# Optimization experiments

Measured on AMD Instinct MI355X. Metric: run time of the kernel, lower is better.

The kernel has to match this reference:

```python
import jax, jax.numpy as jnp
import numpy as np

N = 50000      # nodes
E = 1_600_000  # edges (avg degree 32)
H = 32         # hidden_dim
ED = 16        # edge_dim
L = 4          # num EGNN layers
F_IN = 23      # prot_in_dim
LN_EPS = 1e-5


def setup_inputs() -> dict:
    key = jax.random.key(0)
    ks = jax.random.split(key, 24)
    s = 0.1  # param init scale
    inp = {
        "node_pos": jax.random.normal(ks[0], (N, 3), jnp.float32) * 10.0,
        "node_feat": jax.random.normal(ks[1], (N, F_IN), jnp.float32),
        "edge_attr": jax.random.normal(ks[2], (E, ED), jnp.float32),
        "proj_w": jax.random.normal(ks[3], (F_IN, H), jnp.float32) * s,
        "proj_b": jnp.zeros((H,), jnp.float32),
        # phi_e: Linear(2H+ED+1 -> H), SiLU, Linear(H -> H)   [stacked over L layers]
        "pe_w1": jax.random.normal(ks[4], (L, 2 * H + ED + 1, H), jnp.float32) * s,
        "pe_b1": jnp.zeros((L, H), jnp.float32),
        "pe_w2": jax.random.normal(ks[5], (L, H, H), jnp.float32) * s,
        "pe_b2": jnp.zeros((L, H), jnp.float32),
        # phi_h: Linear(2H -> H), SiLU, Linear(H -> H)
        "ph_w1": jax.random.normal(ks[6], (L, 2 * H, H), jnp.float32) * s,
        "ph_b1": jnp.zeros((L, H), jnp.float32),
        "ph_w2": jax.random.normal(ks[7], (L, H, H), jnp.float32) * s,
        "ph_b2": jnp.zeros((L, H), jnp.float32),
        # phi_x: Linear(H -> H), SiLU, Linear(H -> 1)
        "px_w1": jax.random.normal(ks[8], (L, H, H), jnp.float32) * s,
        "px_b1": jnp.zeros((L, H), jnp.float32),
        "px_w2": jax.random.normal(ks[9], (L, H, 1), jnp.float32) * s,
        "px_b2": jnp.zeros((L, 1), jnp.float32),
        # LayerNorm per layer
        "ln_g": jnp.ones((L, H), jnp.float32),
        "ln_b": jnp.zeros((L, H), jnp.float32),
        "edge_index": jax.random.randint(ks[10], (2, E), 0, N, dtype=jnp.int32),
    }
    return inp


def _mlp2(x, w1, b1, w2, b2):
    # Linear -> SiLU -> Linear (dropout=0 / eval mode)
    return jax.nn.silu(x @ w1 + b1) @ w2 + b2


def _layernorm(x, g, b):
    mu = jnp.mean(x, axis=-1, keepdims=True)
    var = jnp.mean(jnp.square(x - mu), axis=-1, keepdims=True)
    return (x - mu) * jax.lax.rsqrt(var + LN_EPS) * g + b


def reference(node_pos, node_feat, edge_attr, proj_w, proj_b,
              pe_w1, pe_b1, pe_w2, pe_b2,
              ph_w1, ph_b1, ph_w2, ph_b2,
              px_w1, px_b1, px_w2, px_b2,
              ln_g, ln_b, edge_index):
    src = edge_index[0]
    dst = edge_index[1]
    n = node_feat.shape[0]

    h = node_feat @ proj_w + proj_b  # (N,H)
    x = node_pos                     # (N,3)

    for l in range(L):
        h_i = h[src]                 # (E,H)
        h_j = h[dst]                 # (E,H)
        x_i = x[src]                 # (E,3)
        x_j = x[dst]                 # (E,3)
        diff = x_j - x_i             # (E,3)
        dist = jnp.sqrt(jnp.sum(diff * diff, axis=-1, keepdims=True) + 1e-09)  # (E,1)

        m_in = jnp.concatenate([h_i, h_j, edge_attr, dist], axis=-1)  # (E, 2H+ED+1)
        m_ij = _mlp2(m_in, pe_w1[l], pe_b1[l], pe_w2[l], pe_b2[l])    # (E,H)

        agg = jax.ops.segment_sum(m_ij, dst, num_segments=n)          # (N,H)
        dh = _mlp2(jnp.concatenate([h, agg], axis=-1),
                   ph_w1[l], ph_b1[l], ph_w2[l], ph_b2[l])            # (N,H)
        h = _layernorm(h + dh, ln_g[l], ln_b[l])

        # coordinate update: x_j += sum_i unit(x_j - x_i) * phi_x(m_ij)
        dir_norm = jnp.linalg.norm(diff, axis=-1, keepdims=True) + 1e-09
        gate = _mlp2(m_ij, px_w1[l], px_b1[l], px_w2[l], px_b2[l])    # (E,1)
        coord_msg = (diff / dir_norm) * gate                          # (E,3)
        dx = jax.ops.segment_sum(coord_msg, dst, num_segments=n)      # (N,3)
        x = x + dx

    return h, x
```

## Files before the change

### kernel.cpp

```cpp
#include <hip/hip_runtime.h>
#include <hip/hip_fp16.h>
#include <math.h>

#define NN 50000
#define NE 1600000
#define H  32
#define ED 16
#define FIN 23
#define NL 4
#define W1ROWS 81
#define CPAD 16
#define LW 19

typedef _Float16 hv2 __attribute__((ext_vector_type(2)));
typedef __fp16   fv2 __attribute__((ext_vector_type(2)));
union H2U { unsigned int u; hv2 h; fv2 f; };
union F4 { float4 v; float f[4]; };

__device__ __forceinline__ unsigned int pack2(float a, float b) {
    H2U r; r.f = __builtin_amdgcn_cvt_pkrtz(a, b);
    return r.u;
}

__device__ __forceinline__ float fdot2f(unsigned int a, unsigned int b, float c) {
    H2U ua, ub; ua.u = a; ub.u = b;
    return __builtin_amdgcn_fdot2(ua.h, ub.h, c, false);
}

__device__ __forceinline__ float silu_f(float v) {
    float e = __expf(-v);
    return v * __builtin_amdgcn_rcpf(1.0f + e);
}

__device__ __forceinline__ void acc4(float hid[H], float4 hv4, const float* __restrict__ w) {
    F4 u; u.v = hv4;
    #pragma unroll
    for (int jj = 0; jj < 4; ++jj) {
        float v = u.f[jj];
        #pragma unroll
        for (int k = 0; k < H; ++k) hid[k] = fmaf(v, w[jj * H + k], hid[k]);
    }
}


__global__ __launch_bounds__(256) void k_prep(
    const float* __restrict__ pe_w1, const float* __restrict__ pe_w2,
    const float* __restrict__ pe_b2,
    const float* __restrict__ px_w1, const float* __restrict__ px_b1,
    unsigned int* __restrict__ w1h, unsigned int* __restrict__ w2xh,
    float* __restrict__ cvec)
{
    __shared__ float w2x[H * H];
    int l = blockIdx.x;
    const float* w2  = pe_w2 + (size_t)l * H * H;
    const float* xw1 = px_w1 + (size_t)l * H * H;
    int tid = threadIdx.x;
    #pragma unroll
    for (int q = 0; q < 4; ++q) {
        int idx = q * 256 + tid;
        int j = idx >> 5, k = idx & 31;
        float acc = 0.0f;
        #pragma unroll
        for (int t = 0; t < H; ++t) acc = fmaf(w2[j * H + t], xw1[t * H + k], acc);
        w2x[idx] = acc;
    }
    __syncthreads();
    #pragma unroll
    for (int q = 0; q < 2; ++q) {
        int i2 = q * 256 + tid;
        int j2 = i2 >> 5, k = i2 & 31;
        w2xh[(size_t)l * 512 + i2] = pack2(w2x[(2*j2) * H + k], w2x[(2*j2+1) * H + k]);
    }
    {
        int j2 = tid >> 5, k = tid & 31;
        const float* w1 = pe_w1 + (size_t)l * W1ROWS * H;
        w1h[(size_t)l * 256 + tid] = pack2(w1[(2*H + 2*j2) * H + k], w1[(2*H + 2*j2+1) * H + k]);
    }
    if (tid < H) {
        float acc = px_b1[l * H + tid];
        const float* b2 = pe_b2 + l * H;
        #pragma unroll
        for (int t = 0; t < H; ++t) acc = fmaf(b2[t], xw1[t * H + tid], acc);
        cvec[l * H + tid] = acc;
    }
}


__global__ __launch_bounds__(256) void k_hist(
    const int* __restrict__ edst, int* __restrict__ cnt, int* __restrict__ rank)
{
    int e = blockIdx.x * 256 + threadIdx.x;
    if (e >= NE) return;
    rank[e] = atomicAdd(&cnt[(size_t)edst[e] * CPAD], 1);
}

__global__ __launch_bounds__(1024) void k_scan(
    const int* __restrict__ cnt, int* __restrict__ rs)
{
    __shared__ int wsum[16];
    __shared__ int s_carry;
    int t = threadIdx.x;
    int lane = t & 63, wid = t >> 6;
    if (t == 0) s_carry = 0;
    __syncthreads();
    for (int base = 0; base < NN; base += 1024) {
        int i = base + t;
        int v = (i < NN) ? cnt[(size_t)i * CPAD] : 0;
        int incl = v;
        #pragma unroll
        for (int off = 1; off < 64; off <<= 1) {
            int u = __shfl_up(incl, off, 64);
            if (lane >= off) incl += u;
        }
        if (lane == 63) wsum[wid] = incl;
        __syncthreads();
        int wpre = 0;
        #pragma unroll
        for (int w = 0; w < 16; ++w) { int ws = wsum[w]; wpre += (w < wid) ? ws : 0; }
        int carry = s_carry;
        if (i < NN) rs[i] = carry + wpre + incl - v;
        __syncthreads();
        if (t == 1023) s_carry = carry + wpre + incl;
        __syncthreads();
    }
    if (t == 0) rs[NN] = s_carry;
}

__global__ __launch_bounds__(256) void k_scatter2(
    const int* __restrict__ esrc, const int* __restrict__ edst,
    const int* __restrict__ rank, const int* __restrict__ rs,
    const float* __restrict__ ea,
    unsigned int* __restrict__ ea_h, unsigned int* __restrict__ sdp)
{
    int e = blockIdx.x * 256 + threadIdx.x;
    if (e >= NE) return;
    int s = esrc[e], d = edst[e];
    int slot = rs[d] + rank[e];
    const float4* src4 = (const float4*)(ea + (size_t)e * ED);
    uint2* dst2 = (uint2*)(ea_h + (size_t)slot * 8);
    #pragma unroll
    for (int j = 0; j < ED / 4; ++j) {
        float4 v = src4[j];
        uint2 o; o.x = pack2(v.x, v.y); o.y = pack2(v.z, v.w);
        dst2[j] = o;
    }
    sdp[slot] = (unsigned int)s | ((unsigned int)d << 16);
}


__global__ __launch_bounds__(256) void proj2(
    const float* __restrict__ feat, const float* __restrict__ pos,
    const float* __restrict__ W, const float* __restrict__ bias,
    const float* __restrict__ pew1,
    float* __restrict__ h, float* __restrict__ a, float* __restrict__ b,
    float4* __restrict__ xp)
{
    int n = blockIdx.x * 256 + threadIdx.x;
    if (n >= NN) return;
    float acc[H];
    #pragma unroll
    for (int k = 0; k < H; ++k) acc[k] = bias[k];
    #pragma unroll 1
    for (int j = 0; j < FIN; ++j) {
        float v = feat[n * FIN + j];
        const float* w = W + j * H;
        #pragma unroll
        for (int k = 0; k < H; ++k) acc[k] = fmaf(v, w[k], acc[k]);
    }
    float4* h4 = (float4*)(h + (size_t)n * H);
    #pragma unroll
    for (int k4 = 0; k4 < H / 4; ++k4) {
        float4 o;
        o.x = acc[4*k4+0]; o.y = acc[4*k4+1]; o.z = acc[4*k4+2]; o.w = acc[4*k4+3];
        h4[k4] = o;
    }
    float pa[H];
    #pragma unroll
    for (int k = 0; k < H; ++k) pa[k] = 0.0f;
    #pragma unroll 1
    for (int j = 0; j < H; ++j) {
        float v = acc[j];
        const float* w = pew1 + j * H;
        #pragma unroll
        for (int k = 0; k < H; ++k) pa[k] = fmaf(v, w[k], pa[k]);
    }
    float4* a4 = (float4*)(a + (size_t)n * H);
    #pragma unroll
    for (int k4 = 0; k4 < H / 4; ++k4) {
        float4 o;
        o.x = pa[4*k4+0]; o.y = pa[4*k4+1]; o.z = pa[4*k4+2]; o.w = pa[4*k4+3];
        a4[k4] = o;
    }
    #pragma unroll
    for (int k = 0; k < H; ++k) pa[k] = 0.0f;
    #pragma unroll 1
    for (int j = 0; j < H; ++j) {
        float v = acc[j];
        const float* w = pew1 + (H + j) * H;
        #pragma unroll
        for (int k = 0; k < H; ++k) pa[k] = fmaf(v, w[k], pa[k]);
    }
    float4* b4 = (float4*)(b + (size_t)n * H);
    #pragma unroll
    for (int k4 = 0; k4 < H / 4; ++k4) {
        float4 o;
        o.x = pa[4*k4+0]; o.y = pa[4*k4+1]; o.z = pa[4*k4+2]; o.w = pa[4*k4+3];
        b4[k4] = o;
    }
    float4 xo;
    xo.x = pos[3*n+0]; xo.y = pos[3*n+1]; xo.z = pos[3*n+2]; xo.w = 0.0f;
    xp[n] = xo;
}


__global__ __launch_bounds__(256) void egnn_edge6(
    const float* __restrict__ a, const float* __restrict__ b,
    const float4* __restrict__ xp,
    const unsigned int* __restrict__ ea_h, const unsigned int* __restrict__ sdp,
    const unsigned int* __restrict__ w1h, const float* __restrict__ b1,
    const float* __restrict__ w1,
    const unsigned int* __restrict__ w2xh, const float* __restrict__ cvec,
    const float* __restrict__ xw2, const float* __restrict__ xb2,
    float* __restrict__ agg, float* __restrict__ dxb)
{
    __shared__ unsigned int ldsu[256 * LW + 4];

    int tid = threadIdx.x;
    int w = tid >> 6, lane = tid & 63;
    int slot = blockIdx.x * 256 + tid;

    unsigned int sd = sdp[slot];
    int s = (int)(sd & 0xffffu), d = (int)(sd >> 16);

    float hid[H];
    const float4* av = (const float4*)(a + (size_t)s * H);
    const float4* bv = (const float4*)(b + (size_t)d * H);
    #pragma unroll
    for (int k4 = 0; k4 < H / 4; ++k4) {
        F4 ua, ub; ua.v = av[k4]; ub.v = bv[k4];
        #pragma unroll
        for (int jj = 0; jj < 4; ++jj)
            hid[4*k4+jj] = b1[4*k4+jj] + ua.f[jj] + ub.f[jj];
    }

    const uint4* ev = (const uint4*)(ea_h + (size_t)slot * 8);
    uint4 e0 = ev[0], e1 = ev[1];
    unsigned int ew[8] = { e0.x, e0.y, e0.z, e0.w, e1.x, e1.y, e1.z, e1.w };
    #pragma unroll 1
    for (int j2 = 0; j2 < 8; ++j2) {
        unsigned int ea2 = ew[j2];
        const unsigned int* wr = w1h + j2 * H;
        #pragma unroll
        for (int k = 0; k < H; ++k) hid[k] = fdot2f(ea2, wr[k], hid[k]);
    }

    float4 xi = xp[s];
    float4 xj = xp[d];
    float d0 = xj.x - xi.x, d1 = xj.y - xi.y, d2 = xj.z - xi.z;
    float sq = d0*d0 + d1*d1 + d2*d2;
    float dist = __builtin_amdgcn_sqrtf(sq + 1e-9f);
    {
        const float* wl = w1 + (2 * H + ED) * H;
        #pragma unroll
        for (int k = 0; k < H; ++k) hid[k] = fmaf(dist, wl[k], hid[k]);
    }

    unsigned int sp[16];
    #pragma unroll
    for (int j2 = 0; j2 < 16; ++j2)
        sp[j2] = pack2(silu_f(hid[2*j2]), silu_f(hid[2*j2+1]));

    float gh[H];
    #pragma unroll
    for (int k = 0; k < H; ++k) gh[k] = cvec[k];
    #pragma unroll 1
    for (int j2 = 0; j2 < 16; ++j2) {
        unsigned int sv = sp[j2];
        const unsigned int* wr = w2xh + j2 * H;
        #pragma unroll
        for (int k = 0; k < H; ++k) gh[k] = fdot2f(sv, wr[k], gh[k]);
    }

    float gate = xb2[0];
    #pragma unroll
    for (int j = 0; j < H; ++j) gate = fmaf(silu_f(gh[j]), xw2[j], gate);
    float scale = gate * __builtin_amdgcn_rcpf(__builtin_amdgcn_sqrtf(sq) + 1e-9f);

    unsigned int* row = &ldsu[tid * LW];
    #pragma unroll
    for (int k2 = 0; k2 < 16; ++k2) row[k2] = sp[k2];
    row[16] = __float_as_uint(d0 * scale);
    row[17] = __float_as_uint(d1 * scale);
    row[18] = __float_as_uint(d2 * scale);

    int dprev = __shfl_up(d, 1, 64);
    bool flag = (lane == 0) || (d != dprev);
    unsigned long long ball = __ballot(flag);

    int half = lane >> 5, col = lane & 31;
    int word = col >> 1, sh = (col & 1) * 16;
    int c = lane & 3, strip = lane >> 2;
    const unsigned int* wrows = &ldsu[(w * 64) * LW];

    unsigned long long cur = ball;
    while (cur) {
        int r0 = (int)__builtin_ctzll(cur);
        unsigned long long nxt = cur & (cur - 1);
        int r1 = nxt ? (int)__builtin_ctzll(nxt) : 64;
        int dseg = __shfl(d, r0, 64);

        float v = 0.0f;
        #pragma unroll 1
        for (int r = r0 + half; r < r1; r += 2) {
            unsigned int u = wrows[r * LW + word];
            v += __half2float(__ushort_as_half((unsigned short)(u >> sh)));
        }
        v += __shfl_xor(v, 32, 64);
        if (lane < 32) unsafeAtomicAdd(&agg[(size_t)dseg * H + col], v);

        float cv = 0.0f;
        #pragma unroll 1
        for (int r = r0 + strip; r < r1; r += 16)
            cv += __uint_as_float(wrows[r * LW + 16 + c]);
        cv += __shfl_xor(cv, 4, 64);
        cv += __shfl_xor(cv, 8, 64);
        cv += __shfl_xor(cv, 16, 64);
        cv += __shfl_xor(cv, 32, 64);
        if (lane < 3) unsafeAtomicAdd(&dxb[(size_t)dseg * 4 + c], cv);

        cur = nxt;
    }
}


__global__ __launch_bounds__(256) void egnn_node6(
    const float* __restrict__ h, float* __restrict__ agg,
    const float4* __restrict__ xin, float* __restrict__ dxb,
    const int* __restrict__ rs,
    const float* __restrict__ ew2, const float* __restrict__ eb2,
    const float* __restrict__ w1, const float* __restrict__ b1,
    const float* __restrict__ w2, const float* __restrict__ b2,
    const float* __restrict__ lng, const float* __restrict__ lnb,
    const float* __restrict__ nxtw1, int last,
    float* __restrict__ hout, float* __restrict__ xout,
    float* __restrict__ aout, float* __restrict__ bout)
{
    int n = blockIdx.x * 256 + threadIdx.x;
    if (n >= NN) return;
    const float4* h4 = (const float4*)(h + (size_t)n * H);
    float4* a4 = (float4*)(agg + (size_t)n * H);

    float degf = (float)(rs[n + 1] - rs[n]);
    float ma[H];
    #pragma unroll
    for (int k = 0; k < H; ++k) ma[k] = degf * eb2[k];
    #pragma unroll 1
    for (int j4 = 0; j4 < H / 4; ++j4)
        acc4(ma, a4[j4], ew2 + (j4 * 4) * H);

    float4 z; z.x = 0.0f; z.y = 0.0f; z.z = 0.0f; z.w = 0.0f;
    #pragma unroll
    for (int j4 = 0; j4 < H / 4; ++j4) a4[j4] = z;

    float hv[H];
    float hid[H];
    #pragma unroll
    for (int k = 0; k < H; ++k) hid[k] = b1[k];
    #pragma unroll 1
    for (int j4 = 0; j4 < H / 4; ++j4) {
        F4 u; u.v = h4[j4];
        #pragma unroll
        for (int jj = 0; jj < 4; ++jj) hv[4*j4+jj] = u.f[jj];
        acc4(hid, u.v, w1 + (j4 * 4) * H);
    }
    #pragma unroll
    for (int j = 0; j < H; ++j) {
        float v = ma[j];
        const float* ww = w1 + (H + j) * H;
        #pragma unroll
        for (int k = 0; k < H; ++k) hid[k] = fmaf(v, ww[k], hid[k]);
    }

    float dh[H];
    #pragma unroll
    for (int k = 0; k < H; ++k) dh[k] = b2[k];
    #pragma unroll
    for (int j = 0; j < H; ++j) {
        float v = silu_f(hid[j]);
        const float* ww = w2 + j * H;
        #pragma unroll
        for (int k = 0; k < H; ++k) dh[k] = fmaf(v, ww[k], dh[k]);
    }

    float y[H];
    float mu = 0.0f;
    #pragma unroll
    for (int k = 0; k < H; ++k) { y[k] = hv[k] + dh[k]; mu += y[k]; }
    mu *= (1.0f / H);
    float var = 0.0f;
    #pragma unroll
    for (int k = 0; k < H; ++k) { float t = y[k] - mu; var += t * t; }
    var *= (1.0f / H);
    float rstd = rsqrtf(var + 1e-5f);

    float hn[H];
    #pragma unroll
    for (int k = 0; k < H; ++k) hn[k] = (y[k] - mu) * rstd * lng[k] + lnb[k];

    float4* ho4 = (float4*)(hout + (size_t)n * H);
    #pragma unroll
    for (int k4 = 0; k4 < H / 4; ++k4) {
        float4 o;
        o.x = hn[4*k4+0]; o.y = hn[4*k4+1]; o.z = hn[4*k4+2]; o.w = hn[4*k4+3];
        ho4[k4] = o;
    }

    float4 xi = xin[n];
    float nx0 = xi.x + dxb[(size_t)n * 4 + 0];
    float nx1 = xi.y + dxb[(size_t)n * 4 + 1];
    float nx2 = xi.z + dxb[(size_t)n * 4 + 2];
    ((float4*)dxb)[n] = z;
    if (last) {
        xout[3*n+0] = nx0; xout[3*n+1] = nx1; xout[3*n+2] = nx2;
    } else {
        float4 o; o.x = nx0; o.y = nx1; o.z = nx2; o.w = 0.0f;
        ((float4*)xout)[n] = o;
    }

    if (!last) {
        float pa[H];
        #pragma unroll
        for (int k = 0; k < H; ++k) pa[k] = 0.0f;
        #pragma unroll 1
        for (int j = 0; j < H; ++j) {
            float v = hn[j];
            const float* ww = nxtw1 + j * H;
            #pragma unroll
            for (int k = 0; k < H; ++k) pa[k] = fmaf(v, ww[k], pa[k]);
        }
        float4* ao4 = (float4*)(aout + (size_t)n * H);
        #pragma unroll
        for (int k4 = 0; k4 < H / 4; ++k4) {
            float4 o;
            o.x = pa[4*k4+0]; o.y = pa[4*k4+1]; o.z = pa[4*k4+2]; o.w = pa[4*k4+3];
            ao4[k4] = o;
        }
        #pragma unroll
        for (int k = 0; k < H; ++k) pa[k] = 0.0f;
        #pragma unroll 1
        for (int j = 0; j < H; ++j) {
            float v = hn[j];
            const float* ww = nxtw1 + (H + j) * H;
            #pragma unroll
            for (int k = 0; k < H; ++k) pa[k] = fmaf(v, ww[k], pa[k]);
        }
        float4* bo4 = (float4*)(bout + (size_t)n * H);
        #pragma unroll
        for (int k4 = 0; k4 < H / 4; ++k4) {
            float4 o;
            o.x = pa[4*k4+0]; o.y = pa[4*k4+1]; o.z = pa[4*k4+2]; o.w = pa[4*k4+3];
            bo4[k4] = o;
        }
    }
}

extern "C" void kernel_launch(void* const* d_in, const int* in_sizes, int n_in,
                              void* d_out, int out_size, void* d_ws, size_t ws_size,
                              hipStream_t stream) {
    const float* node_pos  = (const float*)d_in[0];
    const float* node_feat = (const float*)d_in[1];
    const float* edge_attr = (const float*)d_in[2];
    const float* proj_w    = (const float*)d_in[3];
    const float* proj_b    = (const float*)d_in[4];
    const float* pe_w1     = (const float*)d_in[5];
    const float* pe_b1     = (const float*)d_in[6];
    const float* pe_w2     = (const float*)d_in[7];
    const float* pe_b2     = (const float*)d_in[8];
    const float* ph_w1     = (const float*)d_in[9];
    const float* ph_b1     = (const float*)d_in[10];
    const float* ph_w2     = (const float*)d_in[11];
    const float* ph_b2     = (const float*)d_in[12];
    const float* px_w1     = (const float*)d_in[13];
    const float* px_b1     = (const float*)d_in[14];
    const float* px_w2     = (const float*)d_in[15];
    const float* px_b2     = (const float*)d_in[16];
    const float* ln_g      = (const float*)d_in[17];
    const float* ln_b      = (const float*)d_in[18];
    const int*   eidx      = (const int*)d_in[19];
    const int*   esrc      = eidx;
    const int*   edst      = eidx + NE;

    float* out_h = (float*)d_out;
    float* out_x = out_h + (size_t)NN * H;

    size_t off = 0;
    unsigned int* ea_h = (unsigned int*)d_ws;   off += (size_t)NE * 8;
    unsigned int* sdp = (unsigned int*)((float*)d_ws + off); off += NE;
    float* abuf = (float*)d_ws + off;          off += (size_t)NN * H;
    float* bbuf = (float*)d_ws + off;          off += (size_t)NN * H;
    float* h_a  = (float*)d_ws + off;          off += (size_t)NN * H;
    float* h_b  = (float*)d_ws + off;          off += (size_t)NN * H;
    float4* xp_a = (float4*)((float*)d_ws + off); off += (size_t)NN * 4;
    float4* xp_b = (float4*)((float*)d_ws + off); off += (size_t)NN * 4;
    float* agg  = (float*)d_ws + off;          off += (size_t)NN * H;
    float* dxb  = (float*)d_ws + off;          off += (size_t)NN * 4;
    unsigned int* w1h  = (unsigned int*)((float*)d_ws + off); off += (size_t)NL * 256;
    unsigned int* w2xh = (unsigned int*)((float*)d_ws + off); off += (size_t)NL * 512;
    float* cvec = (float*)d_ws + off;          off += (size_t)NL * H;
    int*   cnt  = (int*)((float*)d_ws + off);  off += (size_t)NN * CPAD;
    int*   rs   = (int*)((float*)d_ws + off);  off += NN + 4;
    int*   rank = (int*)((float*)d_ws + off);  off += NE;

    dim3 nblk((NN + 255) / 256), eblk(NE / 256);

    hipMemsetAsync(cnt, 0, (size_t)NN * CPAD * sizeof(int), stream);
    hipMemsetAsync(agg, 0, (size_t)NN * (H + 4) * sizeof(float), stream);
    k_hist<<<eblk, 256, 0, stream>>>(edst, cnt, rank);
    k_scan<<<1, 1024, 0, stream>>>(cnt, rs);
    k_scatter2<<<eblk, 256, 0, stream>>>(esrc, edst, rank, rs, edge_attr, ea_h, sdp);
    k_prep<<<dim3(NL), 256, 0, stream>>>(pe_w1, pe_w2, pe_b2, px_w1, px_b1, w1h, w2xh, cvec);

    proj2<<<nblk, 256, 0, stream>>>(node_feat, node_pos, proj_w, proj_b, pe_w1,
                                    h_a, abuf, bbuf, xp_a);

    const float* hcur = h_a;
    const float4* xcur = xp_a;
    float* hbufs[2] = { h_b, h_a };
    float4* xbufs[2] = { xp_b, xp_a };

    for (int l = 0; l < NL; ++l) {
        egnn_edge6<<<eblk, 256, 0, stream>>>(abuf, bbuf, xcur, ea_h, sdp,
            w1h + (size_t)l * 256, pe_b1 + l * H,
            pe_w1 + (size_t)l * W1ROWS * H,
            w2xh + (size_t)l * 512, cvec + l * H,
            px_w2 + (size_t)l * H,  px_b2 + l,
            agg, dxb);
        int last = (l == NL - 1);
        float* ho = last ? out_h : hbufs[l & 1];
        float* xo = last ? out_x : (float*)xbufs[l & 1];
        const float* nxtw1 = last ? pe_w1 : (pe_w1 + (size_t)(l + 1) * W1ROWS * H);
        egnn_node6<<<nblk, 256, 0, stream>>>(hcur, agg, xcur, dxb, rs,
            pe_w2 + (size_t)l * H * H, pe_b2 + l * H,
            ph_w1 + (size_t)l * 2 * H * H, ph_b1 + l * H,
            ph_w2 + (size_t)l * H * H,     ph_b2 + l * H,
            ln_g + l * H, ln_b + l * H,
            nxtw1, last, ho, xo, abuf, bbuf);
        hcur = ho;
        xcur = xbufs[l & 1];
    }
}
```

Measured before the change: 1.005 ms.

## Parallelize CSR prefix scan across blocks and fold edge bias into node projections

Replaces the single-block serial prefix scan over node degree counts with a three-stage multi-block scan, and computes scatter slots via atomic cursors instead of stored per-edge ranks. This removes a long serialized single-workgroup kernel and the rank buffer's write and read. The first-layer edge MLP bias is folded into the per-node precomputed vector so each edge skips one add per hidden unit. Edge ordering within a destination segment stays nondeterministic, as before.

```diff
diff --git a/kernel.cpp b/kernel.cpp
--- a/kernel.cpp
+++ b/kernel.cpp
@@ -11,6 +11,7 @@
 #define W1ROWS 81
 #define CPAD 16
 #define LW 19
+#define NBLK 196
 
 typedef _Float16 hv2 __attribute__((ext_vector_type(2)));
 typedef __fp16   fv2 __attribute__((ext_vector_type(2)));
@@ -87,55 +88,77 @@
 
 
 __global__ __launch_bounds__(256) void k_hist(
-    const int* __restrict__ edst, int* __restrict__ cnt, int* __restrict__ rank)
+    const int* __restrict__ edst, int* __restrict__ cnt)
 {
     int e = blockIdx.x * 256 + threadIdx.x;
     if (e >= NE) return;
-    rank[e] = atomicAdd(&cnt[(size_t)edst[e] * CPAD], 1);
-}
-
-__global__ __launch_bounds__(1024) void k_scan(
-    const int* __restrict__ cnt, int* __restrict__ rs)
-{
-    __shared__ int wsum[16];
-    __shared__ int s_carry;
+    atomicAdd(&cnt[(size_t)edst[e] * CPAD], 1);
+}
+
+__global__ __launch_bounds__(256) void k_scan_a(
+    const int* __restrict__ cnt, int* __restrict__ rs, int* __restrict__ bsum)
+{
+    __shared__ int ws[4];
     int t = threadIdx.x;
-    int lane = t & 63, wid = t >> 6;
-    if (t == 0) s_carry = 0;
+    int lane = t & 63, wv = t >> 6;
+    int i = blockIdx.x * 256 + t;
+    int v = (i < NN) ? cnt[(size_t)i * CPAD] : 0;
+    int incl = v;
+    #pragma unroll
+    for (int off = 1; off < 64; off <<= 1) {
+        int u = __shfl_up(incl, off, 64);
+        if (lane >= off) incl += u;
+    }
+    if (lane == 63) ws[wv] = incl;
     __syncthreads();
-    for (int base = 0; base < NN; base += 1024) {
-        int i = base + t;
-        int v = (i < NN) ? cnt[(size_t)i * CPAD] : 0;
-        int incl = v;
-        #pragma unroll
-        for (int off = 1; off < 64; off <<= 1) {
-            int u = __shfl_up(incl, off, 64);
-            if (lane >= off) incl += u;
-        }
-        if (lane == 63) wsum[wid] = incl;
-        __syncthreads();
-        int wpre = 0;
-        #pragma unroll
-        for (int w = 0; w < 16; ++w) { int ws = wsum[w]; wpre += (w < wid) ? ws : 0; }
-        int carry = s_carry;
-        if (i < NN) rs[i] = carry + wpre + incl - v;
-        __syncthreads();
-        if (t == 1023) s_carry = carry + wpre + incl;
-        __syncthreads();
-    }
-    if (t == 0) rs[NN] = s_carry;
-}
-
-__global__ __launch_bounds__(256) void k_scatter2(
+    int wpre = 0;
+    #pragma unroll
+    for (int w = 0; w < 4; ++w) { int s = ws[w]; wpre += (w < wv) ? s : 0; }
+    if (i < NN) rs[i] = wpre + incl - v;
+    if (t == 255) bsum[blockIdx.x] = wpre + incl;
+}
+
+__global__ __launch_bounds__(256) void k_scan_b(
+    const int* __restrict__ bsum, int* __restrict__ boff, int* __restrict__ rs)
+{
+    __shared__ int ws[4];
+    int t = threadIdx.x;
+    int lane = t & 63, wv = t >> 6;
+    int v = (t < NBLK) ? bsum[t] : 0;
+    int incl = v;
+    #pragma unroll
+    for (int off = 1; off < 64; off <<= 1) {
+        int u = __shfl_up(incl, off, 64);
+        if (lane >= off) incl += u;
+    }
+    if (lane == 63) ws[wv] = incl;
+    __syncthreads();
+    int wpre = 0;
+    #pragma unroll
+    for (int w = 0; w < 4; ++w) { int s = ws[w]; wpre += (w < wv) ? s : 0; }
+    if (t < NBLK) boff[t] = wpre + incl - v;
+    if (t == 255) rs[NN] = wpre + incl;
+}
+
+__global__ __launch_bounds__(256) void k_scan_c(
+    int* __restrict__ rs, const int* __restrict__ boff, int* __restrict__ cursor)
+{
+    int i = blockIdx.x * 256 + threadIdx.x;
+    if (i >= NN) return;
+    int r = rs[i] + boff[blockIdx.x];
+    rs[i] = r;
+    cursor[i] = r;
+}
+
+__global__ __launch_bounds__(256) void k_scatter3(
     const int* __restrict__ esrc, const int* __restrict__ edst,
-    const int* __restrict__ rank, const int* __restrict__ rs,
-    const float* __restrict__ ea,
+    int* __restrict__ cursor, const float* __restrict__ ea,
     unsigned int* __restrict__ ea_h, unsigned int* __restrict__ sdp)
 {
     int e = blockIdx.x * 256 + threadIdx.x;
     if (e >= NE) return;
     int s = esrc[e], d = edst[e];
-    int slot = rs[d] + rank[e];
+    int slot = atomicAdd(&cursor[d], 1);
     const float4* src4 = (const float4*)(ea + (size_t)e * ED);
     uint2* dst2 = (uint2*)(ea_h + (size_t)slot * 8);
     #pragma unroll
@@ -151,7 +174,7 @@
 __global__ __launch_bounds__(256) void proj2(
     const float* __restrict__ feat, const float* __restrict__ pos,
     const float* __restrict__ W, const float* __restrict__ bias,
-    const float* __restrict__ pew1,
+    const float* __restrict__ pew1, const float* __restrict__ eb1,
     float* __restrict__ h, float* __restrict__ a, float* __restrict__ b,
     float4* __restrict__ xp)
 {
@@ -176,7 +199,7 @@
     }
     float pa[H];
     #pragma unroll
-    for (int k = 0; k < H; ++k) pa[k] = 0.0f;
+    for (int k = 0; k < H; ++k) pa[k] = eb1[k];
     #pragma unroll 1
     for (int j = 0; j < H; ++j) {
         float v = acc[j];
@@ -213,11 +236,11 @@
 }
 
 
-__global__ __launch_bounds__(256) void egnn_edge6(
+__global__ __launch_bounds__(256) void egnn_edge7(
     const float* __restrict__ a, const float* __restrict__ b,
     const float4* __restrict__ xp,
     const unsigned int* __restrict__ ea_h, const unsigned int* __restrict__ sdp,
-    const unsigned int* __restrict__ w1h, const float* __restrict__ b1,
+    const unsigned int* __restrict__ w1h,
     const float* __restrict__ w1,
     const unsigned int* __restrict__ w2xh, const float* __restrict__ cvec,
     const float* __restrict__ xw2, const float* __restrict__ xb2,
@@ -240,7 +263,7 @@
         F4 ua, ub; ua.v = av[k4]; ub.v = bv[k4];
         #pragma unroll
         for (int jj = 0; jj < 4; ++jj)
-            hid[4*k4+jj] = b1[4*k4+jj] + ua.f[jj] + ub.f[jj];
+            hid[4*k4+jj] = ua.f[jj] + ub.f[jj];
     }
 
     const uint4* ev = (const uint4*)(ea_h + (size_t)slot * 8);
@@ -333,7 +356,7 @@
 }
 
 
-__global__ __launch_bounds__(256) void egnn_node6(
+__global__ __launch_bounds__(256) void egnn_node7(
     const float* __restrict__ h, float* __restrict__ agg,
     const float4* __restrict__ xin, float* __restrict__ dxb,
     const int* __restrict__ rs,
@@ -341,7 +364,7 @@
     const float* __restrict__ w1, const float* __restrict__ b1,
     const float* __restrict__ w2, const float* __restrict__ b2,
     const float* __restrict__ lng, const float* __restrict__ lnb,
-    const float* __restrict__ nxtw1, int last,
+    const float* __restrict__ nxtw1, const float* __restrict__ nxtb1, int last,
     float* __restrict__ hout, float* __restrict__ xout,
     float* __restrict__ aout, float* __restrict__ bout)
 {
@@ -430,7 +453,7 @@
     if (!last) {
         float pa[H];
         #pragma unroll
-        for (int k = 0; k < H; ++k) pa[k] = 0.0f;
+        for (int k = 0; k < H; ++k) pa[k] = nxtb1[k];
         #pragma unroll 1
         for (int j = 0; j < H; ++j) {
             float v = hn[j];
@@ -509,18 +532,22 @@
     float* cvec = (float*)d_ws + off;          off += (size_t)NL * H;
     int*   cnt  = (int*)((float*)d_ws + off);  off += (size_t)NN * CPAD;
     int*   rs   = (int*)((float*)d_ws + off);  off += NN + 4;
-    int*   rank = (int*)((float*)d_ws + off);  off += NE;
-
-    dim3 nblk((NN + 255) / 256), eblk(NE / 256);
+    int*   cursor = (int*)((float*)d_ws + off); off += NN;
+    int*   bsum = (int*)((float*)d_ws + off);  off += 256;
+    int*   boff = (int*)((float*)d_ws + off);  off += 256;
+
+    dim3 nblk(NBLK), eblk(NE / 256);
 
     hipMemsetAsync(cnt, 0, (size_t)NN * CPAD * sizeof(int), stream);
     hipMemsetAsync(agg, 0, (size_t)NN * (H + 4) * sizeof(float), stream);
-    k_hist<<<eblk, 256, 0, stream>>>(edst, cnt, rank);
-    k_scan<<<1, 1024, 0, stream>>>(cnt, rs);
-    k_scatter2<<<eblk, 256, 0, stream>>>(esrc, edst, rank, rs, edge_attr, ea_h, sdp);
+    k_hist<<<eblk, 256, 0, stream>>>(edst, cnt);
+    k_scan_a<<<nblk, 256, 0, stream>>>(cnt, rs, bsum);
+    k_scan_b<<<1, 256, 0, stream>>>(bsum, boff, rs);
+    k_scan_c<<<nblk, 256, 0, stream>>>(rs, boff, cursor);
+    k_scatter3<<<eblk, 256, 0, stream>>>(esrc, edst, cursor, edge_attr, ea_h, sdp);
     k_prep<<<dim3(NL), 256, 0, stream>>>(pe_w1, pe_w2, pe_b2, px_w1, px_b1, w1h, w2xh, cvec);
 
-    proj2<<<nblk, 256, 0, stream>>>(node_feat, node_pos, proj_w, proj_b, pe_w1,
+    proj2<<<nblk, 256, 0, stream>>>(node_feat, node_pos, proj_w, proj_b, pe_w1, pe_b1,
                                     h_a, abuf, bbuf, xp_a);
 
     const float* hcur = h_a;
@@ -529,8 +556,8 @@
     float4* xbufs[2] = { xp_b, xp_a };
 
     for (int l = 0; l < NL; ++l) {
-        egnn_edge6<<<eblk, 256, 0, stream>>>(abuf, bbuf, xcur, ea_h, sdp,
-            w1h + (size_t)l * 256, pe_b1 + l * H,
+        egnn_edge7<<<eblk, 256, 0, stream>>>(abuf, bbuf, xcur, ea_h, sdp,
+            w1h + (size_t)l * 256,
             pe_w1 + (size_t)l * W1ROWS * H,
             w2xh + (size_t)l * 512, cvec + l * H,
             px_w2 + (size_t)l * H,  px_b2 + l,
@@ -539,12 +566,13 @@
         float* ho = last ? out_h : hbufs[l & 1];
         float* xo = last ? out_x : (float*)xbufs[l & 1];
         const float* nxtw1 = last ? pe_w1 : (pe_w1 + (size_t)(l + 1) * W1ROWS * H);
-        egnn_node6<<<nblk, 256, 0, stream>>>(hcur, agg, xcur, dxb, rs,
+        const float* nxtb1 = last ? pe_b1 : (pe_b1 + (l + 1) * H);
+        egnn_node7<<<nblk, 256, 0, stream>>>(hcur, agg, xcur, dxb, rs,
             pe_w2 + (size_t)l * H * H, pe_b2 + l * H,
             ph_w1 + (size_t)l * 2 * H * H, ph_b1 + l * H,
             ph_w2 + (size_t)l * H * H,     ph_b2 + l * H,
             ln_g + l * H, ln_b + l * H,
-            nxtw1, last, ho, xo, abuf, bbuf);
+            nxtw1, nxtb1, last, ho, xo, abuf, bbuf);
         hcur = ho;
         xcur = xbufs[l & 1];
     }
```

After: 959.6 us. 1.05x faster.
